# Optimization experiments

Hardware: AMD Instinct MI355X
Metric: run time of the kernel (lower is better)

Reference implementation:

```python
import jax, jax.numpy as jnp
import numpy as np
from jax import lax

R = 1
K = 2 * R + 1
C = 16
NF = 4  # identity + 3 random filters
HID = 128
FIRE_RATE = 0.5
STEP_SIZE = 1.0
NEG_SLOPE = 0.01


def _circ_pad(a, r):
    return jnp.pad(a, ((0, 0), (0, 0), (r, r), (r, r)), mode='wrap')


def _make_filters(key):
    # identity filter
    ident = jnp.zeros((K, K), jnp.float32).at[R, R].set(1.0)
    ks = jax.random.split(key, NF - 1)
    rand = []
    for k in ks:
        f = jax.random.normal(k, (K,), jnp.float32)
        f = (f + f[::-1]) / 2.0
        f = jnp.outer(f, f)
        f = f - f.mean()
        f = f.at[R, R].set(0.0)
        f = f / (f.size - 1)
        rand.append(f)
    return jnp.stack([ident] + rand)  # [NF, K, K]


def setup_inputs() -> dict:
    key = jax.random.key(0)
    k1, k2, k3, k4, k5 = jax.random.split(key, 5)
    B, H, W = 32, 128, 128
    x = jax.random.normal(k1, (B, C, H, W), jnp.float32)
    rand_mask = jax.random.uniform(k2, (B, 1, H, W), jnp.float32)
    filters = _make_filters(k3)
    fan_in1 = C * NF
    gain = float(np.sqrt(2.0 / (1.0 + 0.01 ** 2)))  # leaky_relu gain
    lim1 = gain * np.sqrt(6.0 / (fan_in1 + HID))
    lim2 = gain * np.sqrt(6.0 / (HID + C))
    W1 = jax.random.uniform(k4, (HID, fan_in1), jnp.float32, -lim1, lim1)
    W2 = jax.random.uniform(k5, (C, HID), jnp.float32, -lim2, lim2)
    b1 = jnp.zeros((HID,), jnp.float32)
    b2 = jnp.zeros((C,), jnp.float32)
    return {"x": x, "rand_mask": rand_mask, "filters": filters,
            "W1": W1, "b1": b1, "W2": W2, "b2": b2}


def _perceive(x, filters):
    # grouped depthwise conv: each of C channels convolved with all NF filters.
    # Torch output channel order: [c0f0..c0f{NF-1}, c1f0, ...]
    kern = jnp.broadcast_to(filters[None], (C, NF, K, K)).reshape(C * NF, 1, K, K)
    xp = _circ_pad(x, R)  # circular pad + VALID conv == torch pad/conv/crop combo
    return lax.conv_general_dilated(
        xp, kern, window_strides=(1, 1), padding='VALID',
        feature_group_count=C,
        dimension_numbers=('NCHW', 'OIHW', 'NCHW'))


def _living_mask(x):
    alpha = x[:, 3:4]
    ap = _circ_pad(alpha, R)
    alive = lax.reduce_window(ap, -jnp.inf, lax.max,
                              (1, 1, K, K), (1, 1, 1, 1), 'VALID') > 0.1
    avg = lax.reduce_window(ap, 0.0, lax.add,
                            (1, 1, K, K), (1, 1, 1, 1), 'VALID') / (K * K)
    return alive & (avg < 0.2)


def reference(x, rand_mask, filters, W1, b1, W2, b2):
    pre_life = _living_mask(x)
    y = _perceive(x, filters)  # [B, C*NF, H, W]
    h = jnp.einsum('bchw,oc->bohw', y, W1) + b1[None, :, None, None]
    h = jnp.where(h >= 0, h, NEG_SLOPE * h)
    dx = (jnp.einsum('bchw,oc->bohw', h, W2) + b2[None, :, None, None]) * STEP_SIZE
    update_mask = (rand_mask <= FIRE_RATE).astype(x.dtype)
    x = x + dx * update_mask
    post_life = _living_mask(x)
    life = (pre_life & post_life).astype(x.dtype)
    return x * life
```

## Files before the change

### kernel.cpp

```cpp
#include <hip/hip_runtime.h>

#define B_   32
#define C_   16
#define H_   128
#define W_   128
#define HW_  (H_ * W_)
#define HID_ 128
#define FIN_ 64
#define NPIX (B_ * HW_)

typedef float    f32x4 __attribute__((ext_vector_type(4)));
typedef _Float16 f16x8 __attribute__((ext_vector_type(8)));
typedef _Float16 f16x2 __attribute__((ext_vector_type(2)));

#define MFMA16(A, Bv, Cv) __builtin_amdgcn_mfma_f32_16x16x32_f16((A), (Bv), (Cv), 0, 0, 0)

static __device__ __forceinline__ f16x2 pkrtz(float a, float b) {
    auto r = __builtin_amdgcn_cvt_pkrtz(a, b);
    f16x2 out;
    __builtin_memcpy(&out, &r, sizeof(out));
    return out;
}
static __device__ __forceinline__ float lo_of(float v) {
    return v - __uint_as_float(__float_as_uint(v) & 0xFFFFE000u);
}

union YU { f16x2 p[4]; f16x8 v; };

__global__ __launch_bounds__(256) void w_pack(
    const float* __restrict__ W1, const float* __restrict__ W2,
    _Float16* __restrict__ w1p, _Float16* __restrict__ w2p)
{
    int t = blockIdx.x * 256 + threadIdx.x;
    if (t < 32 * 512) {
        int frag = t >> 9, rem = t & 511, l = rem >> 3, j = rem & 7;
        int nt = frag >> 2, kc = (frag >> 1) & 1, s = frag & 1;
        int o = nt * 16 + (l & 15);
        int k = kc * 32 + 16 * (j >> 2) + 4 * (l >> 4) + (j & 3);
        float v = W1[o * FIN_ + k];
        _Float16 hi = (_Float16)v;
        _Float16 lo = (_Float16)(v - (float)hi);
        w1p[t] = s ? lo : hi;
    } else if (t < 32 * 512 + 8 * 512) {
        int u = t - 32 * 512;
        int frag = u >> 9, rem = u & 511, l = rem >> 3, j = rem & 7;
        int kc2 = frag >> 1, s = frag & 1;
        int ch = l & 15;
        int o = kc2 * 32 + 16 * (j >> 2) + 4 * (l >> 4) + (j & 3);
        float v = W2[ch * HID_ + o];
        _Float16 hi = (_Float16)v;
        _Float16 lo = (_Float16)(v - (float)hi);
        w2p[u] = s ? lo : hi;
    }
}

__global__ __launch_bounds__(256) void ca_step(
    const float* __restrict__ x,
    const float* __restrict__ rmask,
    const float* __restrict__ filt,
    const _Float16* __restrict__ w1p,
    const float* __restrict__ b1,
    const _Float16* __restrict__ w2p,
    const float* __restrict__ b2,
    float* __restrict__ out,
    float* __restrict__ alpha_new,
    float* __restrict__ pre_life)
{
    int lane = threadIdx.x & 63, wv = threadIdx.x >> 6;
    int g = lane >> 4, li = lane & 15;
    const f16x8* w1f = (const f16x8*)w1p;
    const f16x8* w2f = (const f16x8*)w2p;

    float fA1 = filt[ 9], fB1 = filt[10];
    float fA2 = filt[18], fB2 = filt[19];
    float fA3 = filt[27], fB3 = filt[28];

    int tb = blockIdx.x * 8 + wv * 2;

    int pxg[2], pixv[2];
    const float* xb_[2];
    int ro[2][3], co[2][3];
    #pragma unroll
    for (int s = 0; s < 2; ++s) {
        int pg = (tb + s) * 16 + li;
        pxg[s] = pg;
        int b = pg >> 14, pix = pg & (HW_ - 1);
        pixv[s] = pix;
        int rr = pix >> 7, cc = pix & (W_ - 1);
        int rm = (rr - 1) & (H_ - 1), rp = (rr + 1) & (H_ - 1);
        int cm = (cc - 1) & (W_ - 1), cp = (cc + 1) & (W_ - 1);
        ro[s][0] = rm * W_; ro[s][1] = rr * W_; ro[s][2] = rp * W_;
        co[s][0] = cm; co[s][1] = cc; co[s][2] = cp;
        xb_[s] = x + (size_t)b * C_ * HW_;
    }

    YU yh[2][2], yl[2][2];
    #pragma unroll
    for (int q = 0; q < 4; ++q) {
        int ch = g + 4 * (q & 1) + 8 * (q >> 1);
        #pragma unroll
        for (int s = 0; s < 2; ++s) {
            const float* xc = xb_[s] + ch * HW_;
            float n[9];
            #pragma unroll
            for (int u = 0; u < 9; ++u) n[u] = xc[ro[s][u / 3] + co[s][u % 3]];
            float cs = (n[0] + n[2]) + (n[6] + n[8]);
            float es = (n[1] + n[3]) + (n[5] + n[7]);
            float y0 = n[4];
            float y1 = fmaf(fA1, cs, fB1 * es);
            float y2 = fmaf(fA2, cs, fB2 * es);
            float y3 = fmaf(fA3, cs, fB3 * es);
            if (q == 0 && g == 3) {
                float mx = n[0];
                #pragma unroll
                for (int u = 1; u < 9; ++u) mx = fmaxf(mx, n[u]);
                float sm = cs + es + n[4];
                pre_life[pxg[s]] =
                    (mx > 0.1f && sm * (1.f / 9.f) < 0.2f) ? 1.f : 0.f;
            }
            int kc = q >> 1, w = (q & 1) * 2;
            yh[s][kc].p[w + 0] = pkrtz(y0, y1);
            yh[s][kc].p[w + 1] = pkrtz(y2, y3);
            yl[s][kc].p[w + 0] = pkrtz(lo_of(y0), lo_of(y1));
            yl[s][kc].p[w + 1] = pkrtz(lo_of(y2), lo_of(y3));
        }
    }

    f32x4 acc2[2] = {{0.f,0.f,0.f,0.f},{0.f,0.f,0.f,0.f}};
    #pragma unroll 1
    for (int kc2 = 0; kc2 < 4; ++kc2) {
        YU Hh[2], Hl[2];
        #pragma unroll
        for (int u = 0; u < 2; ++u) {
            int nt = kc2 * 2 + u;
            f32x4 aA[2] = {{0.f,0.f,0.f,0.f},{0.f,0.f,0.f,0.f}};
            f32x4 aB[2] = {{0.f,0.f,0.f,0.f},{0.f,0.f,0.f,0.f}};
            {
                f16x8 wh = w1f[((nt * 2 + 0) * 2 + 0) * 64 + lane];
                f16x8 wl = w1f[((nt * 2 + 0) * 2 + 1) * 64 + lane];
                aA[0] = MFMA16(wh, yh[0][0].v, aA[0]);
                aA[1] = MFMA16(wh, yh[1][0].v, aA[1]);
                aA[0] = MFMA16(wh, yl[0][0].v, aA[0]);
                aA[1] = MFMA16(wh, yl[1][0].v, aA[1]);
                aA[0] = MFMA16(wl, yh[0][0].v, aA[0]);
                aA[1] = MFMA16(wl, yh[1][0].v, aA[1]);
            }
            {
                f16x8 wh = w1f[((nt * 2 + 1) * 2 + 0) * 64 + lane];
                f16x8 wl = w1f[((nt * 2 + 1) * 2 + 1) * 64 + lane];
                aB[0] = MFMA16(wh, yh[0][1].v, aB[0]);
                aB[1] = MFMA16(wh, yh[1][1].v, aB[1]);
                aB[0] = MFMA16(wh, yl[0][1].v, aB[0]);
                aB[1] = MFMA16(wh, yl[1][1].v, aB[1]);
                aB[0] = MFMA16(wl, yh[0][1].v, aB[0]);
                aB[1] = MFMA16(wl, yh[1][1].v, aB[1]);
            }
            float4 bq = *(const float4*)(b1 + nt * 16 + 4 * g);
            #pragma unroll
            for (int s = 0; s < 2; ++s) {
                float h0 = (aA[s][0] + aB[s][0]) + bq.x;
                float h1 = (aA[s][1] + aB[s][1]) + bq.y;
                float h2 = (aA[s][2] + aB[s][2]) + bq.z;
                float h3 = (aA[s][3] + aB[s][3]) + bq.w;
                h0 = fmaxf(h0, 0.01f * h0);
                h1 = fmaxf(h1, 0.01f * h1);
                h2 = fmaxf(h2, 0.01f * h2);
                h3 = fmaxf(h3, 0.01f * h3);
                Hh[s].p[u * 2 + 0] = pkrtz(h0, h1);
                Hh[s].p[u * 2 + 1] = pkrtz(h2, h3);
                Hl[s].p[u * 2 + 0] = pkrtz(lo_of(h0), lo_of(h1));
                Hl[s].p[u * 2 + 1] = pkrtz(lo_of(h2), lo_of(h3));
            }
        }
        f16x8 w2h = w2f[(kc2 * 2 + 0) * 64 + lane];
        f16x8 w2l = w2f[(kc2 * 2 + 1) * 64 + lane];
        acc2[0] = MFMA16(w2h, Hh[0].v, acc2[0]);
        acc2[1] = MFMA16(w2h, Hh[1].v, acc2[1]);
        acc2[0] = MFMA16(w2h, Hl[0].v, acc2[0]);
        acc2[1] = MFMA16(w2h, Hl[1].v, acc2[1]);
        acc2[0] = MFMA16(w2l, Hh[0].v, acc2[0]);
        acc2[1] = MFMA16(w2l, Hh[1].v, acc2[1]);
    }

    float4 b2q = *(const float4*)(b2 + 4 * g);
    #pragma unroll
    for (int s = 0; s < 2; ++s) {
        int b = pxg[s] >> 14;
        float um = (rmask[pxg[s]] <= 0.5f) ? 1.f : 0.f;
        float bb[4] = { b2q.x, b2q.y, b2q.z, b2q.w };
        float aval = 0.f;
        #pragma unroll
        for (int t = 0; t < 4; ++t) {
            int ch = 4 * g + t;
            float xv = xb_[s][ch * HW_ + pixv[s]];
            float ov = xv + (acc2[s][t] + bb[t]) * um;
            out[(size_t)b * C_ * HW_ + ch * HW_ + pixv[s]] = ov;
            if (t == 3) aval = ov;
        }
        if (g == 0) alpha_new[pxg[s]] = aval;
    }
}

__global__ __launch_bounds__(256) void ca_mask(
    const float* __restrict__ alpha_new,
    const float* __restrict__ pre_life,
    float* __restrict__ out)
{
    int tid = blockIdx.x * blockDim.x + threadIdx.x;
    if (tid >= NPIX) return;
    int b   = tid >> 14;
    int pix = tid & (HW_ - 1);
    int r   = pix >> 7;
    int c   = pix & (W_ - 1);

    int rm = (r - 1) & (H_ - 1), rp = (r + 1) & (H_ - 1);
    int cm = (c - 1) & (W_ - 1), cp = (c + 1) & (W_ - 1);
    int off[9] = { rm * W_ + cm, rm * W_ + c, rm * W_ + cp,
                   r  * W_ + cm, r  * W_ + c, r  * W_ + cp,
                   rp * W_ + cm, rp * W_ + c, rp * W_ + cp };

    const float* ab = alpha_new + (size_t)b * HW_;
    float mx = -1e30f, sm = 0.f;
    #pragma unroll
    for (int t = 0; t < 9; ++t) {
        float v = ab[off[t]];
        mx = fmaxf(mx, v);
        sm += v;
    }
    bool post = (mx > 0.1f) && ((sm * (1.0f / 9.0f)) < 0.2f);
    bool life = post && (pre_life[tid] > 0.5f);
    if (!life) {
        float* ob = out + (size_t)b * C_ * HW_ + pix;
        #pragma unroll
        for (int ch = 0; ch < C_; ++ch) ob[ch * HW_] = 0.f;
    }
}

extern "C" void kernel_launch(void* const* d_in, const int* in_sizes, int n_in,
                              void* d_out, int out_size, void* d_ws, size_t ws_size,
                              hipStream_t stream)
{
    const float* x     = (const float*)d_in[0];
    const float* rmask = (const float*)d_in[1];
    const float* filt  = (const float*)d_in[2];
    const float* W1    = (const float*)d_in[3];
    const float* b1    = (const float*)d_in[4];
    const float* W2    = (const float*)d_in[5];
    const float* b2    = (const float*)d_in[6];
    float* out = (float*)d_out;

    float* alpha_new = (float*)d_ws;
    float* pre_life  = alpha_new + NPIX;
    _Float16* w1p    = (_Float16*)(pre_life + NPIX);
    _Float16* w2p    = w1p + 32 * 512;

    w_pack<<<dim3(80), dim3(256), 0, stream>>>(W1, W2, w1p, w2p);
    ca_step<<<dim3(NPIX / 128), dim3(256), 0, stream>>>(
        x, rmask, filt, w1p, b1, w2p, b2, out, alpha_new, pre_life);
    ca_mask<<<dim3(NPIX / 256), dim3(256), 0, stream>>>(alpha_new, pre_life, out);
}
```

Measured before the change: 71.33 us.

## Process four pixel tiles per wave with block swizzle and merged accumulators

Each wave now handles 64 contiguous pixels in one row (four 16-pixel tiles) instead of two tiles, and the grid is halved. This lets each weight fragment load feed four MFMAs instead of two. A block-index swizzle spreads consecutive blocks across XCDs/rows, and the two partial accumulators for layer 1 are merged into one chain. It raises register pressure (yh/yl/Hh/Hl doubled) and lengthens the serial MFMA dependency chain, which could reduce occupancy.

```diff
diff --git a/kernel.cpp b/kernel.cpp
--- a/kernel.cpp
+++ b/kernel.cpp
@@ -71,51 +71,61 @@
     const f16x8* w1f = (const f16x8*)w1p;
     const f16x8* w2f = (const f16x8*)w2p;
 
+    int bid = blockIdx.x;
+    int swz = (bid & 7) * 256 + (bid >> 3);
+
     float fA1 = filt[ 9], fB1 = filt[10];
     float fA2 = filt[18], fB2 = filt[19];
     float fA3 = filt[27], fB3 = filt[28];
 
-    int tb = blockIdx.x * 8 + wv * 2;
-
-    int pxg[2], pixv[2];
-    const float* xb_[2];
-    int ro[2][3], co[2][3];
-    #pragma unroll
-    for (int s = 0; s < 2; ++s) {
-        int pg = (tb + s) * 16 + li;
-        pxg[s] = pg;
-        int b = pg >> 14, pix = pg & (HW_ - 1);
-        pixv[s] = pix;
-        int rr = pix >> 7, cc = pix & (W_ - 1);
-        int rm = (rr - 1) & (H_ - 1), rp = (rr + 1) & (H_ - 1);
-        int cm = (cc - 1) & (W_ - 1), cp = (cc + 1) & (W_ - 1);
-        ro[s][0] = rm * W_; ro[s][1] = rr * W_; ro[s][2] = rp * W_;
-        co[s][0] = cm; co[s][1] = cc; co[s][2] = cp;
-        xb_[s] = x + (size_t)b * C_ * HW_;
-    }
-
-    YU yh[2][2], yl[2][2];
+    int tb   = swz * 16 + wv * 4;
+    int pg0  = tb * 16;
+    int b    = pg0 >> 14;
+    int pix0 = pg0 & (HW_ - 1);
+    int rr   = pix0 >> 7;
+    int cbase = pix0 & (W_ - 1);
+
+    int rm = (rr - 1) & (H_ - 1), rp = (rr + 1) & (H_ - 1);
+    int roff[3] = { rm * W_, rr * W_, rp * W_ };
+    const float* xb = x + (size_t)b * C_ * HW_;
+
+    int col[4], colm[4], colp[4], pixv[4];
+    #pragma unroll
+    for (int s = 0; s < 4; ++s) {
+        col[s]  = cbase + s * 16 + li;
+        colm[s] = (col[s] - 1) & (W_ - 1);
+        colp[s] = (col[s] + 1) & (W_ - 1);
+        pixv[s] = rr * W_ + col[s];
+    }
+
+    YU yh[4][2], yl[4][2];
     #pragma unroll
     for (int q = 0; q < 4; ++q) {
         int ch = g + 4 * (q & 1) + 8 * (q >> 1);
-        #pragma unroll
-        for (int s = 0; s < 2; ++s) {
-            const float* xc = xb_[s] + ch * HW_;
-            float n[9];
+        const float* xc = xb + ch * HW_;
+        float n[4][9];
+        #pragma unroll
+        for (int s = 0; s < 4; ++s) {
             #pragma unroll
-            for (int u = 0; u < 9; ++u) n[u] = xc[ro[s][u / 3] + co[s][u % 3]];
-            float cs = (n[0] + n[2]) + (n[6] + n[8]);
-            float es = (n[1] + n[3]) + (n[5] + n[7]);
-            float y0 = n[4];
+            for (int u = 0; u < 9; ++u) {
+                int cw = (u % 3 == 0) ? colm[s] : ((u % 3 == 1) ? col[s] : colp[s]);
+                n[s][u] = xc[roff[u / 3] + cw];
+            }
+        }
+        #pragma unroll
+        for (int s = 0; s < 4; ++s) {
+            float cs = (n[s][0] + n[s][2]) + (n[s][6] + n[s][8]);
+            float es = (n[s][1] + n[s][3]) + (n[s][5] + n[s][7]);
+            float y0 = n[s][4];
             float y1 = fmaf(fA1, cs, fB1 * es);
             float y2 = fmaf(fA2, cs, fB2 * es);
             float y3 = fmaf(fA3, cs, fB3 * es);
             if (q == 0 && g == 3) {
-                float mx = n[0];
-                #pragma unroll
-                for (int u = 1; u < 9; ++u) mx = fmaxf(mx, n[u]);
-                float sm = cs + es + n[4];
-                pre_life[pxg[s]] =
+                float mx = n[s][0];
+                #pragma unroll
+                for (int u = 1; u < 9; ++u) mx = fmaxf(mx, n[s][u]);
+                float sm = cs + es + n[s][4];
+                pre_life[b * HW_ + pixv[s]] =
                     (mx > 0.1f && sm * (1.f / 9.f) < 0.2f) ? 1.f : 0.f;
             }
             int kc = q >> 1, w = (q & 1) * 2;
@@ -126,42 +136,43 @@
         }
     }
 
-    f32x4 acc2[2] = {{0.f,0.f,0.f,0.f},{0.f,0.f,0.f,0.f}};
+    f32x4 acc2[4] = {{0.f,0.f,0.f,0.f},{0.f,0.f,0.f,0.f},
+                     {0.f,0.f,0.f,0.f},{0.f,0.f,0.f,0.f}};
     #pragma unroll 1
     for (int kc2 = 0; kc2 < 4; ++kc2) {
-        YU Hh[2], Hl[2];
+        YU Hh[4], Hl[4];
         #pragma unroll
         for (int u = 0; u < 2; ++u) {
             int nt = kc2 * 2 + u;
-            f32x4 aA[2] = {{0.f,0.f,0.f,0.f},{0.f,0.f,0.f,0.f}};
-            f32x4 aB[2] = {{0.f,0.f,0.f,0.f},{0.f,0.f,0.f,0.f}};
+            f32x4 a1[4] = {{0.f,0.f,0.f,0.f},{0.f,0.f,0.f,0.f},
+                           {0.f,0.f,0.f,0.f},{0.f,0.f,0.f,0.f}};
             {
                 f16x8 wh = w1f[((nt * 2 + 0) * 2 + 0) * 64 + lane];
                 f16x8 wl = w1f[((nt * 2 + 0) * 2 + 1) * 64 + lane];
-                aA[0] = MFMA16(wh, yh[0][0].v, aA[0]);
-                aA[1] = MFMA16(wh, yh[1][0].v, aA[1]);
-                aA[0] = MFMA16(wh, yl[0][0].v, aA[0]);
-                aA[1] = MFMA16(wh, yl[1][0].v, aA[1]);
-                aA[0] = MFMA16(wl, yh[0][0].v, aA[0]);
-                aA[1] = MFMA16(wl, yh[1][0].v, aA[1]);
+                #pragma unroll
+                for (int s = 0; s < 4; ++s) a1[s] = MFMA16(wh, yh[s][0].v, a1[s]);
+                #pragma unroll
+                for (int s = 0; s < 4; ++s) a1[s] = MFMA16(wh, yl[s][0].v, a1[s]);
+                #pragma unroll
+                for (int s = 0; s < 4; ++s) a1[s] = MFMA16(wl, yh[s][0].v, a1[s]);
             }
             {
                 f16x8 wh = w1f[((nt * 2 + 1) * 2 + 0) * 64 + lane];
                 f16x8 wl = w1f[((nt * 2 + 1) * 2 + 1) * 64 + lane];
-                aB[0] = MFMA16(wh, yh[0][1].v, aB[0]);
-                aB[1] = MFMA16(wh, yh[1][1].v, aB[1]);
-                aB[0] = MFMA16(wh, yl[0][1].v, aB[0]);
-                aB[1] = MFMA16(wh, yl[1][1].v, aB[1]);
-                aB[0] = MFMA16(wl, yh[0][1].v, aB[0]);
-                aB[1] = MFMA16(wl, yh[1][1].v, aB[1]);
+                #pragma unroll
+                for (int s = 0; s < 4; ++s) a1[s] = MFMA16(wh, yh[s][1].v, a1[s]);
+                #pragma unroll
+                for (int s = 0; s < 4; ++s) a1[s] = MFMA16(wh, yl[s][1].v, a1[s]);
+                #pragma unroll
+                for (int s = 0; s < 4; ++s) a1[s] = MFMA16(wl, yh[s][1].v, a1[s]);
             }
             float4 bq = *(const float4*)(b1 + nt * 16 + 4 * g);
             #pragma unroll
-            for (int s = 0; s < 2; ++s) {
-                float h0 = (aA[s][0] + aB[s][0]) + bq.x;
-                float h1 = (aA[s][1] + aB[s][1]) + bq.y;
-                float h2 = (aA[s][2] + aB[s][2]) + bq.z;
-                float h3 = (aA[s][3] + aB[s][3]) + bq.w;
+            for (int s = 0; s < 4; ++s) {
+                float h0 = a1[s][0] + bq.x;
+                float h1 = a1[s][1] + bq.y;
+                float h2 = a1[s][2] + bq.z;
+                float h3 = a1[s][3] + bq.w;
                 h0 = fmaxf(h0, 0.01f * h0);
                 h1 = fmaxf(h1, 0.01f * h1);
                 h2 = fmaxf(h2, 0.01f * h2);
@@ -174,30 +185,29 @@
         }
         f16x8 w2h = w2f[(kc2 * 2 + 0) * 64 + lane];
         f16x8 w2l = w2f[(kc2 * 2 + 1) * 64 + lane];
-        acc2[0] = MFMA16(w2h, Hh[0].v, acc2[0]);
-        acc2[1] = MFMA16(w2h, Hh[1].v, acc2[1]);
-        acc2[0] = MFMA16(w2h, Hl[0].v, acc2[0]);
-        acc2[1] = MFMA16(w2h, Hl[1].v, acc2[1]);
-        acc2[0] = MFMA16(w2l, Hh[0].v, acc2[0]);
-        acc2[1] = MFMA16(w2l, Hh[1].v, acc2[1]);
+        #pragma unroll
+        for (int s = 0; s < 4; ++s) acc2[s] = MFMA16(w2h, Hh[s].v, acc2[s]);
+        #pragma unroll
+        for (int s = 0; s < 4; ++s) acc2[s] = MFMA16(w2h, Hl[s].v, acc2[s]);
+        #pragma unroll
+        for (int s = 0; s < 4; ++s) acc2[s] = MFMA16(w2l, Hh[s].v, acc2[s]);
     }
 
     float4 b2q = *(const float4*)(b2 + 4 * g);
     #pragma unroll
-    for (int s = 0; s < 2; ++s) {
-        int b = pxg[s] >> 14;
-        float um = (rmask[pxg[s]] <= 0.5f) ? 1.f : 0.f;
+    for (int s = 0; s < 4; ++s) {
+        float um = (rmask[b * HW_ + pixv[s]] <= 0.5f) ? 1.f : 0.f;
         float bb[4] = { b2q.x, b2q.y, b2q.z, b2q.w };
         float aval = 0.f;
         #pragma unroll
         for (int t = 0; t < 4; ++t) {
             int ch = 4 * g + t;
-            float xv = xb_[s][ch * HW_ + pixv[s]];
+            float xv = xb[ch * HW_ + pixv[s]];
             float ov = xv + (acc2[s][t] + bb[t]) * um;
             out[(size_t)b * C_ * HW_ + ch * HW_ + pixv[s]] = ov;
             if (t == 3) aval = ov;
         }
-        if (g == 0) alpha_new[pxg[s]] = aval;
+        if (g == 0) alpha_new[b * HW_ + pixv[s]] = aval;
     }
 }
 
@@ -255,7 +265,7 @@
     _Float16* w2p    = w1p + 32 * 512;
 
     w_pack<<<dim3(80), dim3(256), 0, stream>>>(W1, W2, w1p, w2p);
-    ca_step<<<dim3(NPIX / 128), dim3(256), 0, stream>>>(
+    ca_step<<<dim3(NPIX / 256), dim3(256), 0, stream>>>(
         x, rmask, filt, w1p, b1, w2p, b2, out, alpha_new, pre_life);
     ca_mask<<<dim3(NPIX / 256), dim3(256), 0, stream>>>(alpha_new, pre_life, out);
 }
```

Measured after the change: 69.33 us. -2.8%, faster.
